# Kernel optimization log

Measured on AMD Instinct MI355X. Metric: run time of the kernel, lower is better.

## Reference

```python
import jax, jax.numpy as jnp
import numpy as np
from jax import lax

B, T, V = 128, 256, 64
HF = 32   # MLP feature-imputation hidden
CTX = 32  # context hidden
HID = 64  # LSTM hidden


def _uniform(k, shape, fan):
    s = 1.0 / np.sqrt(fan)
    return jax.random.uniform(k, shape, jnp.float32, -s, s)


def setup_inputs():
    key = jax.random.key(0)
    ks = jax.random.split(key, 40)
    values = jax.random.normal(ks[0], (B, T, V), jnp.float32)
    masks = (jax.random.uniform(ks[1], (B, T, V)) > 0.3).astype(jnp.float32)
    deltas = jax.random.uniform(ks[2], (B, T, V), jnp.float32) * 5.0
    lengths = jax.random.randint(ks[3], (B,), T // 2, T + 1)
    min_vals = jnp.min(values, axis=1, keepdims=True)
    max_vals = jnp.max(values, axis=1, keepdims=True)
    D_in = 2 * V + 2 * CTX
    return dict(
        lengths=lengths, values=values, masks=masks, deltas=deltas,
        min_vals=min_vals, max_vals=max_vals,
        W_decay=_uniform(ks[4], (V, V), V), b_decay=_uniform(ks[5], (V,), V),
        W_feat=_uniform(ks[6], (V, HF, V), V), b_feat=_uniform(ks[7], (V, HF), V),
        W_nl1=_uniform(ks[8], (HF, HF), HF), b_nl1=_uniform(ks[9], (HF,), HF),
        W_nl2=_uniform(ks[10], (1, HF), HF), b_nl2=_uniform(ks[11], (1,), HF),
        Wc1=_uniform(ks[12], (2 * CTX, 3 * V + 1), 3 * V + 1), bc1=_uniform(ks[13], (2 * CTX,), 3 * V + 1),
        Wc2=_uniform(ks[14], (CTX, 2 * CTX), 2 * CTX), bc2=_uniform(ks[15], (CTX,), 2 * CTX),
        W_ih_g=_uniform(ks[16], (3 * CTX, 2 * V), CTX), W_hh_g=_uniform(ks[17], (3 * CTX, CTX), CTX),
        b_ih_g=_uniform(ks[18], (3 * CTX,), CTX), b_hh_g=_uniform(ks[19], (3 * CTX,), CTX),
        W_init=_uniform(ks[20], (2 * HID, 2 * CTX), 2 * CTX), b_init=_uniform(ks[21], (2 * HID,), 2 * CTX),
        W_ih_f=_uniform(ks[22], (4 * HID, D_in), HID), W_hh_f=_uniform(ks[23], (4 * HID, HID), HID),
        b_ih_f=_uniform(ks[24], (4 * HID,), HID), b_hh_f=_uniform(ks[25], (4 * HID,), HID),
        W_ih_b=_uniform(ks[26], (4 * HID, D_in), HID), W_hh_b=_uniform(ks[27], (4 * HID, HID), HID),
        b_ih_b=_uniform(ks[28], (4 * HID,), HID), b_hh_b=_uniform(ks[29], (4 * HID,), HID),
        W_ri=_uniform(ks[30], (V, 2 * HID), 2 * HID), b_ri=_uniform(ks[31], (V,), 2 * HID),
        W_fu=_uniform(ks[32], (V, 2 * V), 2 * V), b_fu=_uniform(ks[33], (V,), 2 * V),
    )


def _gru(x, h, Wih, Whh, bih, bhh):
    gi = x @ Wih.T + bih
    gh = h @ Whh.T + bhh
    ir, iz, inn = jnp.split(gi, 3, axis=-1)
    hr, hz, hn = jnp.split(gh, 3, axis=-1)
    r = jax.nn.sigmoid(ir + hr)
    z = jax.nn.sigmoid(iz + hz)
    n = jnp.tanh(inn + r * hn)
    return (1.0 - z) * n + z * h


def _lstm(x, h, c, Wih, Whh, bih, bhh):
    g = x @ Wih.T + bih + h @ Whh.T + bhh
    i, f, gg, o = jnp.split(g, 4, axis=-1)
    c = jax.nn.sigmoid(f) * c + jax.nn.sigmoid(i) * jnp.tanh(gg)
    h = jax.nn.sigmoid(o) * jnp.tanh(c)
    return h, c


def _forward(lengths, values, masks, deltas, min_vals, max_vals,
             W_decay, b_decay, W_feat, b_feat, W_nl1, b_nl1, W_nl2, b_nl2,
             Wc1, bc1, Wc2, bc2, W_ih_g, W_hh_g, b_ih_g, b_hh_g,
             W_init, b_init, W_ih_f, W_hh_f, b_ih_f, b_hh_f,
             W_ih_b, W_hh_b, b_ih_b, b_hh_b, W_ri, b_ri, W_fu, b_fu):
    Bb, Tt, Vv = values.shape
    lf = lengths.astype(jnp.float32)
    pad = (jnp.arange(Tt)[None, :] + 1 <= lengths[:, None]).astype(jnp.float32)  # [B,T]

    msum = masks.sum(axis=1)                       # [B,V] observation counts
    means = values.sum(axis=1) / msum
    var = ((values - means[:, None, :]) ** 2).sum(axis=1) / (msum - 1.0)
    stdev = jnp.sqrt(var)
    missing = 1.0 - msum / lf[:, None]
    stats = jnp.concatenate([lf[:, None], means, stdev, missing], axis=1)  # [B,3V+1]

    mmn = jnp.maximum(max_vals - min_vals, 1e-8)   # [B,1,V]
    nv = (values - min_vals) / mmn
    nmeans = (means - min_vals[:, 0, :]) / mmn[:, 0, :]

    # last-observation-carried-forward x_prime
    nv_tm = jnp.swapaxes(nv, 0, 1)   # [T,B,V]
    m_tm = jnp.swapaxes(masks, 0, 1)

    def pstep(xp, xm):
        x_prev, m_prev = xm
        xp = m_prev * x_prev + (1.0 - m_prev) * xp
        return xp, xp
    _, xp_rest = lax.scan(pstep, nv_tm[0], (nv_tm[:-1], m_tm[:-1]))
    x_prime = jnp.swapaxes(jnp.concatenate([nv_tm[:1], xp_rest], axis=0), 0, 1)

    # InputTemporalDecay: F.linear(d, W*I, b) == d * diag(W) + b
    gamma = jnp.exp(-jax.nn.relu(deltas * jnp.diag(W_decay) + b_decay))
    x_decay = gamma * x_prime + (1.0 - gamma) * nmeans[:, None, :]
    x_complete = masks * nv + (1.0 - masks) * x_decay

    # context vectors
    ctx_mlp = jax.nn.relu(stats @ Wc1.T + bc1) @ Wc2.T + bc2  # [B,CTX]
    x_rnn_tm = jnp.swapaxes(jnp.concatenate([x_complete, masks], axis=-1), 0, 1)  # [T,B,2V]
    pad_tm = jnp.swapaxes(pad, 0, 1)[:, :, None]
    h0 = jnp.zeros((Bb, W_hh_g.shape[1]), values.dtype)

    def gstep(carry, inp):
        h, hn = carry
        x_t, p_t = inp
        h = _gru(x_t, h, W_ih_g, W_hh_g, b_ih_g, b_hh_g)
        hn = p_t * h + (1.0 - p_t) * hn
        return (h, hn), None
    (_, ctx_rnn), _ = lax.scan(gstep, (h0, h0), (x_rnn_tm, pad_tm))
    context = jnp.concatenate([ctx_mlp, ctx_rnn], axis=1)  # [B,2*CTX]

    hinit = context @ W_init.T + b_init  # [B,2H]
    cinit = jnp.tanh(hinit)
    Hh = hinit.shape[1] // 2
    hf0, hb0 = hinit[:, :Hh], hinit[:, Hh:]
    cf0, cb0 = cinit[:, :Hh], cinit[:, Hh:]

    ctx_bt = jnp.broadcast_to(context[:, None, :], (Bb, Tt, context.shape[1]))
    rnn_in_tm = jnp.swapaxes(jnp.concatenate([x_complete, masks, ctx_bt], axis=-1), 0, 1)  # [T,B,D]

    def fstep(carry, x):
        h, c = _lstm(x, carry[0], carry[1], W_ih_f, W_hh_f, b_ih_f, b_hh_f)
        return (h, c), h
    _, hf_rest = lax.scan(fstep, (hf0, cf0), rnn_in_tm[:-1])
    hf_all = jnp.concatenate([hf0[None], hf_rest], axis=0)  # [T,B,H]

    def bstep(carry, x):
        h, c = _lstm(x, carry[0], carry[1], W_ih_b, W_hh_b, b_ih_b, b_hh_b)
        return (h, c), h
    _, hb_rest = lax.scan(bstep, (hb0, cb0), rnn_in_tm[1:][::-1])  # t = T-1 .. 1
    hb_all = jnp.concatenate([hb0[None], hb_rest], axis=0)[::-1]   # time-aligned

    h_cat = jnp.concatenate([hf_all, hb_all], axis=-1)  # [T,B,2H]
    rnn_imp = jnp.swapaxes(h_cat @ W_ri.T + b_ri, 0, 1)  # [B,T,V]

    # per-variable masked feature imputation (no self-connection)
    eye = jnp.eye(Vv, dtype=values.dtype)
    Wm = W_feat * (1.0 - eye[:, None, :])                 # [V,HF,V]
    hidden = jnp.einsum('btv,ghv->btgh', x_complete, Wm) + b_feat  # [B,T,V,HF]
    z = jax.nn.relu(hidden) @ W_nl1.T + b_nl1
    feat_imp = (jax.nn.relu(z) @ W_nl2.T + b_nl2)[..., 0]  # [B,T,V]

    beta = jax.nn.sigmoid(jnp.concatenate([gamma, masks], axis=-1) @ W_fu.T + b_fu)
    final_imp = beta * feat_imp + (1.0 - beta) * rnn_imp

    # unnormalize all three estimates; stack as [3,B,T,V]
    out = jnp.stack([rnn_imp, feat_imp, final_imp], axis=0) * mmn[None] + min_vals[None]
    return out


def reference(lengths, values, masks, deltas, min_vals, max_vals,
              W_decay, b_decay, W_feat, b_feat, W_nl1, b_nl1, W_nl2, b_nl2,
              Wc1, bc1, Wc2, bc2, W_ih_g, W_hh_g, b_ih_g, b_hh_g,
              W_init, b_init, W_ih_f, W_hh_f, b_ih_f, b_hh_f,
              W_ih_b, W_hh_b, b_ih_b, b_hh_b, W_ri, b_ri, W_fu, b_fu):
    return _forward(lengths, values, masks, deltas, min_vals, max_vals,
                    W_decay, b_decay, W_feat, b_feat, W_nl1, b_nl1, W_nl2, b_nl2,
                    Wc1, bc1, Wc2, bc2, W_ih_g, W_hh_g, b_ih_g, b_hh_g,
                    W_init, b_init, W_ih_f, W_hh_f, b_ih_f, b_hh_f,
                    W_ih_b, W_hh_b, b_ih_b, b_hh_b, W_ri, b_ri, W_fu, b_fu)
```

## Files before the change

### kernel.cpp

```cpp
#include <hip/hip_runtime.h>
#include <hip/hip_fp16.h>

static constexpr int NB = 128;
static constexpr int NT = 256;
static constexpr int NV = 64;
static constexpr int NBT = NB * NT;
static constexpr int NBTV = NBT * NV;

typedef __attribute__((ext_vector_type(8))) short short8;
typedef __attribute__((ext_vector_type(4))) float f32x4;
typedef __attribute__((ext_vector_type(4))) float fvec4;

__device__ __forceinline__ void wave_lds_fence() {
    __builtin_amdgcn_sched_barrier(0);
    asm volatile("s_waitcnt lgkmcnt(0)" ::: "memory");
    __builtin_amdgcn_sched_barrier(0);
}

__device__ __forceinline__ void block_sync_lds() {
    __builtin_amdgcn_sched_barrier(0);
    asm volatile("s_waitcnt lgkmcnt(0)" ::: "memory");
    __builtin_amdgcn_s_barrier();
    asm volatile("" ::: "memory");
    __builtin_amdgcn_sched_barrier(0);
}

__device__ __forceinline__ unsigned short f2bf(float x) {
    unsigned int u = __float_as_uint(x);
    return (unsigned short)((u + 0x7FFFu + ((u >> 16) & 1u)) >> 16);
}
__device__ __forceinline__ float bf2f(unsigned short b) {
    return __uint_as_float(((unsigned int)b) << 16);
}
__device__ __forceinline__ unsigned short f2h(float x) {
    union { _Float16 h; unsigned short u; } c; c.h = (_Float16)x; return c.u;
}
__device__ __forceinline__ float fsigm(float x) {
    return __builtin_amdgcn_rcpf(1.0f + __expf(-x));
}
__device__ __forceinline__ float ftanh(float x) {
    return 1.0f - 2.0f * __builtin_amdgcn_rcpf(1.0f + __expf(2.0f * x));
}

__device__ __forceinline__ short8 pack8(float4 a, float4 b) {
    short8 r;
    r[0] = (short)f2bf(a.x); r[1] = (short)f2bf(a.y); r[2] = (short)f2bf(a.z); r[3] = (short)f2bf(a.w);
    r[4] = (short)f2bf(b.x); r[5] = (short)f2bf(b.y); r[6] = (short)f2bf(b.z); r[7] = (short)f2bf(b.w);
    return r;
}

__device__ __forceinline__ void dot4(float4& acc, const float4 wv, const float4 xv) {
    acc.x = fmaf(wv.x, xv.x, acc.x);
    acc.y = fmaf(wv.y, xv.y, acc.y);
    acc.z = fmaf(wv.z, xv.z, acc.z);
    acc.w = fmaf(wv.w, xv.w, acc.w);
}

__global__ __launch_bounds__(256) void k_prep(
    const float* __restrict__ Wf, const float* __restrict__ Wihf,
    const float* __restrict__ Wihb, const float* __restrict__ Wihg,
    const float* __restrict__ Whhf, const float* __restrict__ Whhb,
    const float* __restrict__ Whhg, const float* __restrict__ Wri,
    const float* __restrict__ Wfu,
    unsigned short* __restrict__ wbf, float* __restrict__ wdiag,
    unsigned short* __restrict__ wgf, unsigned short* __restrict__ wgb,
    unsigned short* __restrict__ wgg,
    unsigned short* __restrict__ whhf_h, unsigned short* __restrict__ whhb_h,
    unsigned short* __restrict__ whhg_h,
    unsigned short* __restrict__ wri_bf, unsigned short* __restrict__ wfu_bf,
    const int* __restrict__ lengths, const float* __restrict__ values,
    const float* __restrict__ masks, const float* __restrict__ minv,
    const float* __restrict__ maxv, float* __restrict__ stats,
    float* __restrict__ mmn_ws, float* __restrict__ nmeans_ws) {
    __shared__ float red[3][4][64];
    int bx = blockIdx.x;
    if (bx < 512) {
        int i = bx * 256 + threadIdx.x;
        if (i < NV * 32 * NV) wbf[i] = f2bf(Wf[i]);
        if (i < 2048) wdiag[i] = bf2f(f2bf(Wf[i * 64 + (i >> 5)]));
        if (i < 32768) {
            int n = i >> 7, k = i & 127;
            wgf[i] = f2bf(Wihf[n * 192 + k]);
            wgb[i] = f2bf(Wihb[n * 192 + k]);
        }
        if (i < 12288) wgg[i] = f2bf(Wihg[i]);
        if (i < 16384) { whhf_h[i] = f2h(Whhf[i]); whhb_h[i] = f2h(Whhb[i]); }
        if (i < 3072) whhg_h[i] = f2h(Whhg[i]);
        if (i < 8192) { wri_bf[i] = f2bf(Wri[i]); wfu_bf[i] = f2bf(Wfu[i]); }
    } else {
        int b = bx - 512; int tid = threadIdx.x;
        int v = tid & 63; int tc = tid >> 6;
        const float* vp = values + (size_t)b * NT * NV;
        const float* mp = masks + (size_t)b * NT * NV;
        float sv = 0.f, sq = 0.f, sm = 0.f;
        for (int t = tc; t < NT; t += 4) {
            float x = vp[t * NV + v]; float m = mp[t * NV + v];
            sv += x; sq += x * x; sm += m;
        }
        red[0][tc][v] = sv; red[1][tc][v] = sq; red[2][tc][v] = sm;
        __syncthreads();
        if (tc == 0) {
            sv = red[0][0][v] + red[0][1][v] + red[0][2][v] + red[0][3][v];
            sq = red[1][0][v] + red[1][1][v] + red[1][2][v] + red[1][3][v];
            sm = red[2][0][v] + red[2][1][v] + red[2][2][v] + red[2][3][v];
            float mean = sv / sm;
            float var = (sq - 2.0f * mean * sv + (float)NT * mean * mean) / (sm - 1.0f);
            var = fmaxf(var, 0.0f);
            float sd = sqrtf(var);
            float lf = (float)lengths[b];
            float miss = 1.0f - sm / lf;
            float mn = minv[b * NV + v]; float mx = maxv[b * NV + v];
            float mm = fmaxf(mx - mn, 1e-8f);
            float* st = stats + b * 256;
            if (v == 0) st[0] = lf;
            st[1 + v] = mean; st[65 + v] = sd; st[129 + v] = miss;
            mmn_ws[b * NV + v] = mm;
            nmeans_ws[b * NV + v] = (mean - mn) / mm;
        }
    }
}

__global__ __launch_bounds__(256) void k_fill(
    const float* __restrict__ values, const float* __restrict__ masks,
    const float* __restrict__ deltas, const float* __restrict__ minv,
    const float* __restrict__ Wd, const float* __restrict__ bd,
    const float* __restrict__ mmn_ws, const float* __restrict__ nmeans_ws,
    float* __restrict__ xcomp, float* __restrict__ gam) {
    int b = blockIdx.x; int tid = threadIdx.x;
    int v = tid & 63; int tc = tid >> 6;
    float mn = minv[b * NV + v];
    float mm = mmn_ws[b * NV + v];
    float nmean = nmeans_ws[b * NV + v];
    float wd = Wd[v * NV + v], bdv = bd[v];
    size_t base = (size_t)b * NT * NV + v;
    __shared__ float lastv[4][64];
    __shared__ int hasf[4][64];
    __shared__ float nv0s[64];
    int t0 = tc * 64;
    float last = 0.f; int has = 0;
    for (int t = t0; t < t0 + 64; t++) {
        float val = values[base + (size_t)t * NV];
        float m = masks[base + (size_t)t * NV];
        float nv = (val - mn) / mm;
        if (m != 0.f) { last = nv; has = 1; }
        if (tc == 0 && t == 0) nv0s[v] = nv;
    }
    lastv[tc][v] = last; hasf[tc][v] = has;
    __syncthreads();
    float xp = nv0s[v];
    for (int q = tc - 1; q >= 0; q--) {
        if (hasf[q][v]) { xp = lastv[q][v]; break; }
    }
    for (int t = t0; t < t0 + 64; t++) {
        size_t i = base + (size_t)t * NV;
        float val = values[i], m = masks[i], d = deltas[i];
        float nv = (val - mn) / mm;
        float g = expf(-fmaxf(fmaf(d, wd, bdv), 0.0f));
        float xd = g * xp + (1.0f - g) * nmean;
        float xc = m * nv + (1.0f - m) * xd;
        xcomp[i] = xc; gam[i] = g;
        xp = (m != 0.f) ? nv : xp;
    }
}

__global__ __launch_bounds__(256) void k_gates_g(
    const float* __restrict__ xcomp, const float* __restrict__ masks,
    const unsigned short* __restrict__ wgg, const float* __restrict__ bihg,
    float* __restrict__ gg) {
    int wave = threadIdx.x >> 6, lane = threadIdx.x & 63;
    int bt0 = blockIdx.x * 64 + wave * 16;
    int r = lane & 15, kc = lane >> 4;
    const float* xr = xcomp + (size_t)(bt0 + r) * NV + kc * 8;
    const float* mr = masks + (size_t)(bt0 + r) * NV + kc * 8;
    short8 af0 = pack8(*(const float4*)(xr), *(const float4*)(xr + 4));
    short8 af1 = pack8(*(const float4*)(xr + 32), *(const float4*)(xr + 36));
    short8 af2 = pack8(*(const float4*)(mr), *(const float4*)(mr + 4));
    short8 af3 = pack8(*(const float4*)(mr + 32), *(const float4*)(mr + 36));
    #pragma unroll 3
    for (int nt = 0; nt < 6; nt++) {
        const unsigned short* w = wgg + (size_t)(nt * 16 + r) * 128 + kc * 8;
        float bias = bihg[nt * 16 + r];
        f32x4 acc = {bias, bias, bias, bias};
        acc = __builtin_amdgcn_mfma_f32_16x16x32_bf16(af0, *(const short8*)(w), acc, 0, 0, 0);
        acc = __builtin_amdgcn_mfma_f32_16x16x32_bf16(af1, *(const short8*)(w + 32), acc, 0, 0, 0);
        acc = __builtin_amdgcn_mfma_f32_16x16x32_bf16(af2, *(const short8*)(w + 64), acc, 0, 0, 0);
        acc = __builtin_amdgcn_mfma_f32_16x16x32_bf16(af3, *(const short8*)(w + 96), acc, 0, 0, 0);
        #pragma unroll
        for (int i = 0; i < 4; i++)
            gg[(size_t)(bt0 + kc * 4 + i) * 96 + nt * 16 + r] = acc[i];
    }
}

#define GRU_STEP(T, GIN) { \
    const int t_ = (T); const int p_ = t_ & 1; \
    int4 raw_[4]; \
    const int4* hp_ = (const int4*)hsg[g][s]; \
    _Pragma("unroll") for (int q = 0; q < 4; q++) raw_[q] = hp_[q]; \
    const __half2* hhv_ = (const __half2*)raw_; \
    __half2 a0_ = zh2, a1_ = zh2, a2_ = zh2, a3_ = zh2; \
    _Pragma("unroll") for (int q = 0; q < 16; q += 4) { \
        a0_ = __hfma2(w2[q],     hhv_[q],     a0_); \
        a1_ = __hfma2(w2[q + 1], hhv_[q + 1], a1_); \
        a2_ = __hfma2(w2[q + 2], hhv_[q + 2], a2_); \
        a3_ = __hfma2(w2[q + 3], hhv_[q + 3], a3_); } \
    __half2 sA_ = __hadd2(__hadd2(a0_, a1_), __hadd2(a2_, a3_)); \
    float d_ = __low2float(sA_) + __high2float(sA_); \
    if (g < 2) { \
        gexg[p_][s][n][g] = GIN + bh + d_; \
    } else { \
        gexg[p_][s][n][2] = bh + d_; \
        gexg[p_][s][n][3] = GIN; \
    } \
    block_sync_lds(); \
    float qx_ = gexg[p_][s][n][0], qy_ = gexg[p_][s][n][1]; \
    float qz_ = gexg[p_][s][n][2], qw_ = gexg[p_][s][n][3]; \
    float rr_ = fsigm(qx_); \
    float zz_ = fsigm(qy_); \
    float nn_ = ftanh(qw_ + rr_ * qz_); \
    float h_ = (1.f - zz_) * nn_ + zz_ * hprev; \
    hprev = h_; \
    if (t_ < len) hn = h_; \
    hsg[g][s][n] = f2h(h_); \
    wave_lds_fence(); \
}

__global__ __launch_bounds__(256, 1) void k_mid(
    const float* __restrict__ gg_t, const int* __restrict__ lengths,
    const unsigned short* __restrict__ whhg_h, const float* __restrict__ bhh,
    float* __restrict__ ctx,
    const float* __restrict__ stats, const float* __restrict__ Wc1,
    const float* __restrict__ bc1, const float* __restrict__ Wc2,
    const float* __restrict__ bc2,
    const float* __restrict__ xcomp, const float* __restrict__ masks,
    const unsigned short* __restrict__ wbf,
    const float* __restrict__ wdiag, const float* __restrict__ bfeat,
    const float* __restrict__ Wnl1, const float* __restrict__ bnl1,
    const float* __restrict__ Wnl2, const float* __restrict__ bnl2,
    float* __restrict__ feat_out,
    const unsigned short* __restrict__ wgf, const unsigned short* __restrict__ wgb,
    float* __restrict__ gf, float* __restrict__ gb) {
    __shared__ __align__(16) unsigned short hsg[3][2][32];
    __shared__ __align__(16) float gexg[2][2][32][5];
    __shared__ __align__(16) float ss[193];
    __shared__ float h1[64];
    __shared__ __align__(16) unsigned short hbs[4][16 * 32];
    __shared__ __align__(16) float ldsx[4][64 * 16];
    __shared__ __align__(16) float fls[4][16 * 65];

    int bx = blockIdx.x;
    int tid = threadIdx.x;

    if (bx < 64) {
        int b0 = bx * 2;
        int g = tid >> 6;
        int lane = tid & 63;
        int s = lane >> 5, n = lane & 31;
        if (g == 3) {
            for (int t = 0; t < NT; t++) block_sync_lds();
            return;
        }
        int b = b0 + s;
        const __half2 zh2 = __float2half2_rn(0.f);
        int4 w4[4];
        {
            const int4* wp = (const int4*)(whhg_h + (size_t)(g * 32 + n) * 32);
            #pragma unroll
            for (int q = 0; q < 4; q++) w4[q] = wp[q];
        }
        const __half2* w2 = (const __half2*)w4;
        float bh = bhh[g * 32 + n];
        int len = lengths[b];
        float hprev = 0.f, hn = 0.f;
        hsg[g][s][n] = f2h(0.f);
        const float* gbase = gg_t + (size_t)b * NT * 96;
        #define GGIDX(T) ((size_t)(T) * 96 + g * 32 + n)
        float gi0 = gbase[GGIDX(0)];
        float gi1 = gbase[GGIDX(1)];
        float gi2 = gbase[GGIDX(2)];
        float gi3 = gbase[GGIDX(3)];
        wave_lds_fence();
        for (int t = 0; t < 252; t += 4) {
            GRU_STEP(t, gi0)
            gi0 = gbase[GGIDX(t + 4)];
            GRU_STEP(t + 1, gi1)
            gi1 = gbase[GGIDX(t + 5)];
            GRU_STEP(t + 2, gi2)
            gi2 = gbase[GGIDX(t + 6)];
            GRU_STEP(t + 3, gi3)
            gi3 = gbase[GGIDX(t + 7)];
        }
        GRU_STEP(252, gi0)
        GRU_STEP(253, gi1)
        GRU_STEP(254, gi2)
        GRU_STEP(255, gi3)
        #undef GGIDX
        if (g == 0) ctx[(b0 + s) * 64 + 32 + n] = hn;
    } else if (bx < 192) {
        if (tid >= 64) return;
        int b = bx - 64;
        ss[tid] = stats[b * 256 + tid];
        ss[64 + tid] = stats[b * 256 + 64 + tid];
        ss[128 + tid] = stats[b * 256 + 128 + tid];
        if (tid == 0) ss[192] = stats[b * 256 + 192];
        wave_lds_fence();
        float acc = bc1[tid];
        const float* w = Wc1 + (size_t)tid * 193;
        for (int k = 0; k < 193; k++) acc = fmaf(w[k], ss[k], acc);
        h1[tid] = fmaxf(acc, 0.f);
        wave_lds_fence();
        if (tid < 32) {
            float a = bc2[tid];
            const float* w2 = Wc2 + tid * 64;
            for (int k = 0; k < 64; k++) a = fmaf(w2[k], h1[k], a);
            ctx[b * 64 + tid] = a;
        }
    } else if (bx < 704) {
        int wave = tid >> 6; int lane = tid & 63;
        int bt0 = (bx - 192) * 64 + wave * 16;
        int r = lane & 15, kc = lane >> 4;
        unsigned short* hbw = hbs[wave];
        float* lx = ldsx[wave];
        float* flw = fls[wave];

        short8 a0, a1;
        {
            const float* xr = xcomp + (size_t)(bt0 + r) * NV + kc * 8;
            a0 = pack8(*(const float4*)(xr), *(const float4*)(xr + 4));
            a1 = pack8(*(const float4*)(xr + 32), *(const float4*)(xr + 36));
        }
        {
            int gc0 = kc * 16;
            const float* xr2 = xcomp + (size_t)(bt0 + r) * NV + gc0;
            #pragma unroll
            for (int e = 0; e < 16; e += 4) {
                float4 p = *(const float4*)(xr2 + e);
                lx[(gc0 + e + 0) * 16 + r] = bf2f(f2bf(p.x));
                lx[(gc0 + e + 1) * 16 + r] = bf2f(f2bf(p.y));
                lx[(gc0 + e + 2) * 16 + r] = bf2f(f2bf(p.z));
                lx[(gc0 + e + 3) * 16 + r] = bf2f(f2bf(p.w));
            }
        }
        short8 wb0, wb1;
        {
            const float* w = Wnl1 + r * 32 + kc * 8;
            wb0 = pack8(*(const float4*)w, *(const float4*)(w + 4));
            const float* w2 = Wnl1 + (16 + r) * 32 + kc * 8;
            wb1 = pack8(*(const float4*)w2, *(const float4*)(w2 + 4));
        }
        float b0i[4], b1i[4], w2a[4], w2b[4];
        #pragma unroll
        for (int i = 0; i < 4; i++) {
            b0i[i] = bnl1[kc * 4 + i];
            b1i[i] = bnl1[16 + kc * 4 + i];
            w2a[i] = Wnl2[kc * 4 + i];
            w2b[i] = Wnl2[16 + kc * 4 + i];
        }
        float bn2 = bnl2[0];
        __builtin_amdgcn_wave_barrier();

        #pragma unroll 2
        for (int g = 0; g < 64; g++) {
            __builtin_amdgcn_wave_barrier();
            float xv[4];
            #pragma unroll
            for (int i = 0; i < 4; i++) xv[i] = lx[g * 16 + kc * 4 + i];
            #pragma unroll
            for (int f = 0; f < 2; f++) {
                int n0 = g * 32 + f * 16;
                const unsigned short* wrow = wbf + (size_t)(n0 + r) * 64;
                short8 b0 = *(const short8*)(wrow + kc * 8);
                short8 b1 = *(const short8*)(wrow + 32 + kc * 8);
                f32x4 acc = {0.f, 0.f, 0.f, 0.f};
                acc = __builtin_amdgcn_mfma_f32_16x16x32_bf16(a0, b0, acc, 0, 0, 0);
                acc = __builtin_amdgcn_mfma_f32_16x16x32_bf16(a1, b1, acc, 0, 0, 0);
                int n = n0 + r;
                float wd = wdiag[n], bs = bfeat[n];
                #pragma unroll
                for (int i = 0; i < 4; i++) {
                    float h = acc[i] - xv[i] * wd + bs;
                    h = fmaxf(h, 0.0f);
                    hbw[(kc * 4 + i) * 32 + f * 16 + r] = f2bf(h);
                }
            }
            __builtin_amdgcn_wave_barrier();
            short8 ah = *(const short8*)(hbw + r * 32 + kc * 8);
            f32x4 zt0 = {0.f, 0.f, 0.f, 0.f}, zt1 = {0.f, 0.f, 0.f, 0.f};
            zt0 = __builtin_amdgcn_mfma_f32_16x16x32_bf16(wb0, ah, zt0, 0, 0, 0);
            zt1 = __builtin_amdgcn_mfma_f32_16x16x32_bf16(wb1, ah, zt1, 0, 0, 0);
            float p = 0.f;
            #pragma unroll
            for (int i = 0; i < 4; i++) {
                p = fmaf(fmaxf(zt0[i] + b0i[i], 0.0f), w2a[i], p);
                p = fmaf(fmaxf(zt1[i] + b1i[i], 0.0f), w2b[i], p);
            }
            p += __shfl_xor(p, 16, 64);
            p += __shfl_xor(p, 32, 64);
            if (lane < 16) flw[lane * 65 + g] = p + bn2;
        }
        __builtin_amdgcn_wave_barrier();
        #pragma unroll
        for (int q = 0; q < 16; q++)
            feat_out[(size_t)(bt0 + q) * NV + lane] = flw[q * 65 + lane];
    } else {
        int wave = tid >> 6, lane = tid & 63;
        int bt0 = (bx - 704) * 64 + wave * 16;
        int r = lane & 15, kc = lane >> 4;
        const float* xr = xcomp + (size_t)(bt0 + r) * NV + kc * 8;
        const float* mr = masks + (size_t)(bt0 + r) * NV + kc * 8;
        short8 af0 = pack8(*(const float4*)(xr), *(const float4*)(xr + 4));
        short8 af1 = pack8(*(const float4*)(xr + 32), *(const float4*)(xr + 36));
        short8 af2 = pack8(*(const float4*)(mr), *(const float4*)(mr + 4));
        short8 af3 = pack8(*(const float4*)(mr + 32), *(const float4*)(mr + 36));
        #pragma unroll 4
        for (int nt = 0; nt < 16; nt++) {
            const unsigned short* w = wgf + (size_t)(nt * 16 + r) * 128 + kc * 8;
            f32x4 acc = {0.f, 0.f, 0.f, 0.f};
            acc = __builtin_amdgcn_mfma_f32_16x16x32_bf16(af0, *(const short8*)(w), acc, 0, 0, 0);
            acc = __builtin_amdgcn_mfma_f32_16x16x32_bf16(af1, *(const short8*)(w + 32), acc, 0, 0, 0);
            acc = __builtin_amdgcn_mfma_f32_16x16x32_bf16(af2, *(const short8*)(w + 64), acc, 0, 0, 0);
            acc = __builtin_amdgcn_mfma_f32_16x16x32_bf16(af3, *(const short8*)(w + 96), acc, 0, 0, 0);
            int col = nt * 16 + r, g = col >> 6, n = col & 63;
            #pragma unroll
            for (int i = 0; i < 4; i++)
                gf[((size_t)(bt0 + kc * 4 + i) * 64 + n) * 4 + g] = acc[i];
        }
        #pragma unroll 4
        for (int nt = 0; nt < 16; nt++) {
            const unsigned short* w = wgb + (size_t)(nt * 16 + r) * 128 + kc * 8;
            f32x4 acc = {0.f, 0.f, 0.f, 0.f};
            acc = __builtin_amdgcn_mfma_f32_16x16x32_bf16(af0, *(const short8*)(w), acc, 0, 0, 0);
            acc = __builtin_amdgcn_mfma_f32_16x16x32_bf16(af1, *(const short8*)(w + 32), acc, 0, 0, 0);
            acc = __builtin_amdgcn_mfma_f32_16x16x32_bf16(af2, *(const short8*)(w + 64), acc, 0, 0, 0);
            acc = __builtin_amdgcn_mfma_f32_16x16x32_bf16(af3, *(const short8*)(w + 96), acc, 0, 0, 0);
            int col = nt * 16 + r, g = col >> 6, n = col & 63;
            #pragma unroll
            for (int i = 0; i < 4; i++)
                gb[((size_t)(bt0 + kc * 4 + i) * 64 + n) * 4 + g] = acc[i];
        }
    }
}

__global__ __launch_bounds__(256) void k_hc(
    const float* __restrict__ ctx, const float* __restrict__ Wi,
    const float* __restrict__ bi, float* __restrict__ hinit,
    const float* __restrict__ Wihf, const float* __restrict__ Wihb,
    const float* __restrict__ bihf, const float* __restrict__ bhhf,
    const float* __restrict__ bihb, const float* __restrict__ bhhb,
    float* __restrict__ ct_out) {
    __shared__ __align__(16) float sc[64];
    int bx = blockIdx.x; int tid = threadIdx.x;
    if (bx < 128) {
        int b = bx; int j = tid;
        if (j < 64) sc[j] = ctx[b * 64 + j];
        __syncthreads();
        if (j < 128) {
            const float4* w = (const float4*)(Wi + (size_t)j * 64);
            const float4* c4 = (const float4*)sc;
            float4 a = {0, 0, 0, 0};
            #pragma unroll
            for (int q = 0; q < 16; q++) dot4(a, w[q], c4[q]);
            hinit[b * 128 + j] = bi[j] + a.x + a.y + a.z + a.w;
        }
    } else {
        int bxx = bx - 128; int dir = bxx >> 7; int b = bxx & 127;
        int col = tid;
        if (col < 64) sc[col] = ctx[b * 64 + col];
        __syncthreads();
        const float* wc = (dir ? Wihb : Wihf) + (size_t)col * 192 + 128;
        float bias = dir ? (bihb[col] + bhhb[col]) : (bihf[col] + bhhf[col]);
        const float4* c4 = (const float4*)sc;
        float4 a = {0, 0, 0, 0};
        #pragma unroll
        for (int q = 0; q < 16; q++) dot4(a, *(const float4*)(wc + q * 4), c4[q]);
        int g = col >> 6, n = col & 63;
        ct_out[((size_t)bxx * 64 + n) * 4 + g] = bias + a.x + a.y + a.z + a.w;
    }
}

#define LSTM_STEP(S, GIN) { \
    const int s_ = (S); const int p_ = s_ & 1; \
    int4 raw_[8]; \
    const int4* hp_ = (const int4*)hs[g]; \
    _Pragma("unroll") for (int q = 0; q < 8; q++) raw_[q] = hp_[q]; \
    const __half2* hhv_ = (const __half2*)raw_; \
    __half2 a0_ = zh2, a1_ = zh2, a2_ = zh2, a3_ = zh2; \
    _Pragma("unroll") for (int q = 0; q < 32; q += 4) { \
        a0_ = __hfma2(w2[q],     hhv_[q],     a0_); \
        a1_ = __hfma2(w2[q + 1], hhv_[q + 1], a1_); \
        a2_ = __hfma2(w2[q + 2], hhv_[q + 2], a2_); \
        a3_ = __hfma2(w2[q + 3], hhv_[q + 3], a3_); } \
    __half2 sA_ = __hadd2(__hadd2(a0_, a1_), __hadd2(a2_, a3_)); \
    float d_ = __low2float(sA_) + __high2float(sA_); \
    gex[p_][n][g] = GIN + ctg + d_; \
    block_sync_lds(); \
    float qx_ = gex[p_][n][0], qy_ = gex[p_][n][1]; \
    float qz_ = gex[p_][n][2], qw_ = gex[p_][n][3]; \
    float ii_ = fsigm(qx_); \
    float ff_ = fsigm(qy_); \
    float gv_ = ftanh(qz_); \
    float oo_ = fsigm(qw_); \
    c = ff_ * c + ii_ * gv_; \
    float hv_ = oo_ * ftanh(c); \
    if (g == 0) { \
        int tout_ = dir ? (NT - 2 - s_) : (s_ + 1); \
        hall[((size_t)b * NT + tout_) * NV + n] = hv_; \
    } \
    hs[g][n] = f2h(hv_); \
    wave_lds_fence(); \
}

__global__ __launch_bounds__(256, 1) void k_lstm(
    const float* __restrict__ gf, const float* __restrict__ gb,
    const float* __restrict__ cterm, const float* __restrict__ hinit,
    const unsigned short* __restrict__ whhf_h, const unsigned short* __restrict__ whhb_h,
    float* __restrict__ out0, float* __restrict__ out1) {
    int bx = blockIdx.x; int dir = bx >> 7; int b = bx & 127;
    int tid = threadIdx.x;
    int g = tid >> 6;
    int n = tid & 63;
    const float* gates = dir ? gb : gf;
    const unsigned short* wsrc = dir ? whhb_h : whhf_h;
    float* hall = dir ? out1 : out0;
    __shared__ __align__(16) unsigned short hs[4][64];
    __shared__ __align__(16) float gex[2][64][5];
    const __half2 zh2 = __float2half2_rn(0.f);
    int4 w4[8];
    {
        const int4* wp = (const int4*)(wsrc + (size_t)(g * 64 + n) * 64);
        #pragma unroll
        for (int q = 0; q < 8; q++) w4[q] = wp[q];
    }
    const __half2* w2 = (const __half2*)w4;
    float ctg = cterm[((size_t)bx * 64 + n) * 4 + g];
    float c;
    {
        float h0 = hinit[b * 128 + dir * 64 + n];
        c = ftanh(h0);
        hs[g][n] = f2h(h0);
        if (g == 0) {
            int t0 = dir ? (NT - 1) : 0;
            hall[((size_t)b * NT + t0) * NV + n] = h0;
        }
    }
    size_t gbase = (size_t)b * NT * 256;
    #define GIDX(S) (gbase + (size_t)(dir ? (NT - 1 - (S)) : (S)) * 256 + n * 4 + g)
    float gi0 = gates[GIDX(0)];
    float gi1 = gates[GIDX(1)];
    float gi2 = gates[GIDX(2)];
    float gi3 = gates[GIDX(3)];
    wave_lds_fence();
    for (int sx = 0; sx < 252; sx += 4) {
        LSTM_STEP(sx, gi0)
        gi0 = gates[GIDX(sx + 4)];
        LSTM_STEP(sx + 1, gi1)
        gi1 = gates[GIDX(sx + 5)];
        LSTM_STEP(sx + 2, gi2)
        gi2 = gates[GIDX(sx + 6)];
        LSTM_STEP(sx + 3, gi3)
        gi3 = gates[GIDX(sx + 7)];
    }
    LSTM_STEP(252, gi0)
    LSTM_STEP(253, gi1)
    LSTM_STEP(254, gi2)
    #undef GIDX
}

__global__ __launch_bounds__(256) void k_post(
    const float* __restrict__ gam, const float* __restrict__ masks,
    const unsigned short* __restrict__ wri_bf, const unsigned short* __restrict__ wfu_bf,
    const float* __restrict__ bri, const float* __restrict__ bfu,
    const float* __restrict__ mmn_ws, const float* __restrict__ minv,
    float* out0, float* out1, float* out2) {
    int wave = threadIdx.x >> 6, lane = threadIdx.x & 63;
    int bt0 = blockIdx.x * 64 + wave * 16;
    int r = lane & 15, kc = lane >> 4;
    int b = bt0 >> 8;
    const float* h0r = out0 + (size_t)(bt0 + r) * NV + kc * 8;
    const float* h1r = out1 + (size_t)(bt0 + r) * NV + kc * 8;
    const float* gr  = gam  + (size_t)(bt0 + r) * NV + kc * 8;
    const float* mr  = masks + (size_t)(bt0 + r) * NV + kc * 8;
    short8 A0 = pack8(*(const float4*)(h0r), *(const float4*)(h0r + 4));
    short8 A1 = pack8(*(const float4*)(h0r + 32), *(const float4*)(h0r + 36));
    short8 A2 = pack8(*(const float4*)(h1r), *(const float4*)(h1r + 4));
    short8 A3 = pack8(*(const float4*)(h1r + 32), *(const float4*)(h1r + 36));
    short8 G0 = pack8(*(const float4*)(gr), *(const float4*)(gr + 4));
    short8 G1 = pack8(*(const float4*)(gr + 32), *(const float4*)(gr + 36));
    short8 M0 = pack8(*(const float4*)(mr), *(const float4*)(mr + 4));
    short8 M1 = pack8(*(const float4*)(mr + 32), *(const float4*)(mr + 36));
    #pragma unroll
    for (int nt = 0; nt < 4; nt++) {
        int n = nt * 16 + r;
        const unsigned short* wr = wri_bf + (size_t)n * 128 + kc * 8;
        const unsigned short* wf = wfu_bf + (size_t)n * 128 + kc * 8;
        float bi = bri[n], bf_ = bfu[n];
        f32x4 racc = {bi, bi, bi, bi};
        f32x4 bacc = {bf_, bf_, bf_, bf_};
        racc = __builtin_amdgcn_mfma_f32_16x16x32_bf16(A0, *(const short8*)(wr), racc, 0, 0, 0);
        racc = __builtin_amdgcn_mfma_f32_16x16x32_bf16(A1, *(const short8*)(wr + 32), racc, 0, 0, 0);
        racc = __builtin_amdgcn_mfma_f32_16x16x32_bf16(A2, *(const short8*)(wr + 64), racc, 0, 0, 0);
        racc = __builtin_amdgcn_mfma_f32_16x16x32_bf16(A3, *(const short8*)(wr + 96), racc, 0, 0, 0);
        bacc = __builtin_amdgcn_mfma_f32_16x16x32_bf16(G0, *(const short8*)(wf), bacc, 0, 0, 0);
        bacc = __builtin_amdgcn_mfma_f32_16x16x32_bf16(G1, *(const short8*)(wf + 32), bacc, 0, 0, 0);
        bacc = __builtin_amdgcn_mfma_f32_16x16x32_bf16(M0, *(const short8*)(wf + 64), bacc, 0, 0, 0);
        bacc = __builtin_amdgcn_mfma_f32_16x16x32_bf16(M1, *(const short8*)(wf + 96), bacc, 0, 0, 0);
        float mm = mmn_ws[b * NV + n], mn = minv[b * NV + n];
        #pragma unroll
        for (int i = 0; i < 4; i++) {
            int row = bt0 + kc * 4 + i;
            size_t idx = (size_t)row * NV + n;
            float rn = racc[i];
            float beta = fsigm(bacc[i]);
            float ft = out2[idx];
            float fin = beta * ft + (1.0f - beta) * rn;
            out0[idx] = fmaf(rn, mm, mn);
            out1[idx] = fmaf(ft, mm, mn);
            out2[idx] = fmaf(fin, mm, mn);
        }
    }
}

extern "C" void kernel_launch(void* const* d_in, const int* in_sizes, int n_in,
                              void* d_out, int out_size, void* d_ws, size_t ws_size,
                              hipStream_t stream) {
    const int*   lengths  = (const int*)d_in[0];
    const float* values   = (const float*)d_in[1];
    const float* masks    = (const float*)d_in[2];
    const float* deltas   = (const float*)d_in[3];
    const float* min_vals = (const float*)d_in[4];
    const float* max_vals = (const float*)d_in[5];
    const float* W_decay  = (const float*)d_in[6];
    const float* b_decay  = (const float*)d_in[7];
    const float* W_feat   = (const float*)d_in[8];
    const float* b_feat   = (const float*)d_in[9];
    const float* W_nl1    = (const float*)d_in[10];
    const float* b_nl1    = (const float*)d_in[11];
    const float* W_nl2    = (const float*)d_in[12];
    const float* b_nl2    = (const float*)d_in[13];
    const float* Wc1      = (const float*)d_in[14];
    const float* bc1      = (const float*)d_in[15];
    const float* Wc2      = (const float*)d_in[16];
    const float* bc2      = (const float*)d_in[17];
    const float* W_ih_g   = (const float*)d_in[18];
    const float* W_hh_g   = (const float*)d_in[19];
    const float* b_ih_g   = (const float*)d_in[20];
    const float* b_hh_g   = (const float*)d_in[21];
    const float* W_init   = (const float*)d_in[22];
    const float* b_init   = (const float*)d_in[23];
    const float* W_ih_f   = (const float*)d_in[24];
    const float* W_hh_f   = (const float*)d_in[25];
    const float* b_ih_f   = (const float*)d_in[26];
    const float* b_hh_f   = (const float*)d_in[27];
    const float* W_ih_b   = (const float*)d_in[28];
    const float* W_hh_b   = (const float*)d_in[29];
    const float* b_ih_b   = (const float*)d_in[30];
    const float* b_hh_b   = (const float*)d_in[31];
    const float* W_ri     = (const float*)d_in[32];
    const float* b_ri     = (const float*)d_in[33];
    const float* W_fu     = (const float*)d_in[34];
    const float* b_fu     = (const float*)d_in[35];

    float* ws = (float*)d_ws;
    float* xcomp  = ws;
    float* gam    = ws + 2097152;
    unsigned short* wri_bf = (unsigned short*)(ws + 4194304);
    unsigned short* wfu_bf = (unsigned short*)(ws + 4198400);
    float* stats  = ws + 6291456;
    float* mmn    = ws + 6324224;
    float* nmeans = ws + 6332416;
    float* ctx    = ws + 6340608;
    float* hinit  = ws + 6348800;
    unsigned short* wbf = (unsigned short*)(ws + 6365184);
    float* wdiag  = ws + 6430720;
    unsigned short* wgf = (unsigned short*)(ws + 6432768);
    unsigned short* wgb = (unsigned short*)(ws + 6449152);
    unsigned short* wgg = (unsigned short*)(ws + 6465536);
    unsigned short* whhf_h = (unsigned short*)(ws + 6471680);
    unsigned short* whhb_h = (unsigned short*)(ws + 6479872);
    unsigned short* whhg_h = (unsigned short*)(ws + 6488064);
    float* cterm  = ws + 6489600;
    float* gates_f = ws + 6555136;
    float* gates_b = ws + 14943744;
    float* gates_g = ws + 23332352;

    float* out0 = (float*)d_out;
    float* out1 = out0 + NBTV;
    float* out2 = out0 + 2 * NBTV;

    k_prep<<<640, 256, 0, stream>>>(W_feat, W_ih_f, W_ih_b, W_ih_g, W_hh_f, W_hh_b, W_hh_g,
                                    W_ri, W_fu,
                                    wbf, wdiag, wgf, wgb, wgg, whhf_h, whhb_h, whhg_h,
                                    wri_bf, wfu_bf,
                                    lengths, values, masks, min_vals, max_vals, stats, mmn, nmeans);
    k_fill<<<NB, 256, 0, stream>>>(values, masks, deltas, min_vals, W_decay, b_decay, mmn, nmeans, xcomp, gam);
    k_gates_g<<<NBT / 64, 256, 0, stream>>>(xcomp, masks, wgg, b_ih_g, gates_g);
    k_mid<<<1216, 256, 0, stream>>>(gates_g, lengths, whhg_h, b_hh_g, ctx,
                                    stats, Wc1, bc1, Wc2, bc2,
                                    xcomp, masks, wbf, wdiag, b_feat, W_nl1, b_nl1, W_nl2, b_nl2, out2,
                                    wgf, wgb, gates_f, gates_b);
    k_hc<<<384, 256, 0, stream>>>(ctx, W_init, b_init, hinit,
                                  W_ih_f, W_ih_b, b_ih_f, b_hh_f, b_ih_b, b_hh_b, cterm);
    k_lstm<<<256, 256, 0, stream>>>(gates_f, gates_b, cterm, hinit, whhf_h, whhb_h, out0, out1);
    k_post<<<NBT / 64, 256, 0, stream>>>(gam, masks, wri_bf, wfu_bf, b_ri, b_fu, mmn, min_vals,
                                         out0, out1, out2);
}
```

Measured before the change: 307.2 us.

## Fold k_hc into LSTM and move half of feature MLP into LSTM launch

Removes the k_hc launch by computing the initial hidden state and context gate term inside each LSTM block. Half of the feature-imputation MLP blocks move from k_mid into extra blocks of the k_lstm grid, so they can fill CUs left idle by the 256 latency-bound LSTM blocks. This cuts one launch and shortens k_mid. The risk is that the larger LDS footprint in k_lstm and block scheduling order could delay the LSTM blocks.

New measurement: 285.4 us. -7.1%, faster.

```diff
diff --git a/kernel.cpp b/kernel.cpp
--- a/kernel.cpp
+++ b/kernel.cpp
@@ -224,6 +224,84 @@
     wave_lds_fence(); \
 }
 
+#define FEAT_BODY(BT0) { \
+    int bt0 = (BT0); \
+    int r = lane & 15, kc = lane >> 4; \
+    unsigned short* hbw = hbs[wave]; \
+    float* lx = ldsx[wave]; \
+    float* flw = fls[wave]; \
+    short8 a0, a1; \
+    { \
+        const float* xr = xcomp + (size_t)(bt0 + r) * NV + kc * 8; \
+        a0 = pack8(*(const float4*)(xr), *(const float4*)(xr + 4)); \
+        a1 = pack8(*(const float4*)(xr + 32), *(const float4*)(xr + 36)); \
+    } \
+    { \
+        int gc0 = kc * 16; \
+        const float* xr2 = xcomp + (size_t)(bt0 + r) * NV + gc0; \
+        _Pragma("unroll") for (int e = 0; e < 16; e += 4) { \
+            float4 p = *(const float4*)(xr2 + e); \
+            lx[(gc0 + e + 0) * 16 + r] = bf2f(f2bf(p.x)); \
+            lx[(gc0 + e + 1) * 16 + r] = bf2f(f2bf(p.y)); \
+            lx[(gc0 + e + 2) * 16 + r] = bf2f(f2bf(p.z)); \
+            lx[(gc0 + e + 3) * 16 + r] = bf2f(f2bf(p.w)); \
+        } \
+    } \
+    short8 wb0, wb1; \
+    { \
+        const float* w = Wnl1 + r * 32 + kc * 8; \
+        wb0 = pack8(*(const float4*)w, *(const float4*)(w + 4)); \
+        const float* w2p = Wnl1 + (16 + r) * 32 + kc * 8; \
+        wb1 = pack8(*(const float4*)w2p, *(const float4*)(w2p + 4)); \
+    } \
+    float b0i[4], b1i[4], w2a[4], w2b[4]; \
+    _Pragma("unroll") for (int i = 0; i < 4; i++) { \
+        b0i[i] = bnl1[kc * 4 + i]; \
+        b1i[i] = bnl1[16 + kc * 4 + i]; \
+        w2a[i] = Wnl2[kc * 4 + i]; \
+        w2b[i] = Wnl2[16 + kc * 4 + i]; \
+    } \
+    float bn2 = bnl2[0]; \
+    __builtin_amdgcn_wave_barrier(); \
+    _Pragma("unroll 2") for (int g = 0; g < 64; g++) { \
+        __builtin_amdgcn_wave_barrier(); \
+        float xv[4]; \
+        _Pragma("unroll") for (int i = 0; i < 4; i++) xv[i] = lx[g * 16 + kc * 4 + i]; \
+        _Pragma("unroll") for (int f = 0; f < 2; f++) { \
+            int n0 = g * 32 + f * 16; \
+            const unsigned short* wrow = wbf + (size_t)(n0 + r) * 64; \
+            short8 b0 = *(const short8*)(wrow + kc * 8); \
+            short8 b1 = *(const short8*)(wrow + 32 + kc * 8); \
+            f32x4 acc = {0.f, 0.f, 0.f, 0.f}; \
+            acc = __builtin_amdgcn_mfma_f32_16x16x32_bf16(a0, b0, acc, 0, 0, 0); \
+            acc = __builtin_amdgcn_mfma_f32_16x16x32_bf16(a1, b1, acc, 0, 0, 0); \
+            int n = n0 + r; \
+            float wd = wdiag[n], bs = bfeat[n]; \
+            _Pragma("unroll") for (int i = 0; i < 4; i++) { \
+                float h = acc[i] - xv[i] * wd + bs; \
+                h = fmaxf(h, 0.0f); \
+                hbw[(kc * 4 + i) * 32 + f * 16 + r] = f2bf(h); \
+            } \
+        } \
+        __builtin_amdgcn_wave_barrier(); \
+        short8 ah = *(const short8*)(hbw + r * 32 + kc * 8); \
+        f32x4 zt0 = {0.f, 0.f, 0.f, 0.f}, zt1 = {0.f, 0.f, 0.f, 0.f}; \
+        zt0 = __builtin_amdgcn_mfma_f32_16x16x32_bf16(wb0, ah, zt0, 0, 0, 0); \
+        zt1 = __builtin_amdgcn_mfma_f32_16x16x32_bf16(wb1, ah, zt1, 0, 0, 0); \
+        float p = 0.f; \
+        _Pragma("unroll") for (int i = 0; i < 4; i++) { \
+            p = fmaf(fmaxf(zt0[i] + b0i[i], 0.0f), w2a[i], p); \
+            p = fmaf(fmaxf(zt1[i] + b1i[i], 0.0f), w2b[i], p); \
+        } \
+        p += __shfl_xor(p, 16, 64); \
+        p += __shfl_xor(p, 32, 64); \
+        if (lane < 16) flw[lane * 65 + g] = p + bn2; \
+    } \
+    __builtin_amdgcn_wave_barrier(); \
+    _Pragma("unroll") for (int q = 0; q < 16; q++) \
+        feat_out[(size_t)(bt0 + q) * NV + lane] = flw[q * 65 + lane]; \
+}
+
 __global__ __launch_bounds__(256, 1) void k_mid(
     const float* __restrict__ gg_t, const int* __restrict__ lengths,
     const unsigned short* __restrict__ whhg_h, const float* __restrict__ bhh,
@@ -314,96 +392,12 @@
             for (int k = 0; k < 64; k++) a = fmaf(w2[k], h1[k], a);
             ctx[b * 64 + tid] = a;
         }
-    } else if (bx < 704) {
+    } else if (bx < 448) {
         int wave = tid >> 6; int lane = tid & 63;
-        int bt0 = (bx - 192) * 64 + wave * 16;
-        int r = lane & 15, kc = lane >> 4;
-        unsigned short* hbw = hbs[wave];
-        float* lx = ldsx[wave];
-        float* flw = fls[wave];
-
-        short8 a0, a1;
-        {
-            const float* xr = xcomp + (size_t)(bt0 + r) * NV + kc * 8;
-            a0 = pack8(*(const float4*)(xr), *(const float4*)(xr + 4));
-            a1 = pack8(*(const float4*)(xr + 32), *(const float4*)(xr + 36));
-        }
-        {
-            int gc0 = kc * 16;
-            const float* xr2 = xcomp + (size_t)(bt0 + r) * NV + gc0;
-            #pragma unroll
-            for (int e = 0; e < 16; e += 4) {
-                float4 p = *(const float4*)(xr2 + e);
-                lx[(gc0 + e + 0) * 16 + r] = bf2f(f2bf(p.x));
-                lx[(gc0 + e + 1) * 16 + r] = bf2f(f2bf(p.y));
-                lx[(gc0 + e + 2) * 16 + r] = bf2f(f2bf(p.z));
-                lx[(gc0 + e + 3) * 16 + r] = bf2f(f2bf(p.w));
-            }
-        }
-        short8 wb0, wb1;
-        {
-            const float* w = Wnl1 + r * 32 + kc * 8;
-            wb0 = pack8(*(const float4*)w, *(const float4*)(w + 4));
-            const float* w2 = Wnl1 + (16 + r) * 32 + kc * 8;
-            wb1 = pack8(*(const float4*)w2, *(const float4*)(w2 + 4));
-        }
-        float b0i[4], b1i[4], w2a[4], w2b[4];
-        #pragma unroll
-        for (int i = 0; i < 4; i++) {
-            b0i[i] = bnl1[kc * 4 + i];
-            b1i[i] = bnl1[16 + kc * 4 + i];
-            w2a[i] = Wnl2[kc * 4 + i];
-            w2b[i] = Wnl2[16 + kc * 4 + i];
-        }
-        float bn2 = bnl2[0];
-        __builtin_amdgcn_wave_barrier();
-
-        #pragma unroll 2
-        for (int g = 0; g < 64; g++) {
-            __builtin_amdgcn_wave_barrier();
-            float xv[4];
-            #pragma unroll
-            for (int i = 0; i < 4; i++) xv[i] = lx[g * 16 + kc * 4 + i];
-            #pragma unroll
-            for (int f = 0; f < 2; f++) {
-                int n0 = g * 32 + f * 16;
-                const unsigned short* wrow = wbf + (size_t)(n0 + r) * 64;
-                short8 b0 = *(const short8*)(wrow + kc * 8);
-                short8 b1 = *(const short8*)(wrow + 32 + kc * 8);
-                f32x4 acc = {0.f, 0.f, 0.f, 0.f};
-                acc = __builtin_amdgcn_mfma_f32_16x16x32_bf16(a0, b0, acc, 0, 0, 0);
-                acc = __builtin_amdgcn_mfma_f32_16x16x32_bf16(a1, b1, acc, 0, 0, 0);
-                int n = n0 + r;
-                float wd = wdiag[n], bs = bfeat[n];
-                #pragma unroll
-                for (int i = 0; i < 4; i++) {
-                    float h = acc[i] - xv[i] * wd + bs;
-                    h = fmaxf(h, 0.0f);
-                    hbw[(kc * 4 + i) * 32 + f * 16 + r] = f2bf(h);
-                }
-            }
-            __builtin_amdgcn_wave_barrier();
-            short8 ah = *(const short8*)(hbw + r * 32 + kc * 8);
-            f32x4 zt0 = {0.f, 0.f, 0.f, 0.f}, zt1 = {0.f, 0.f, 0.f, 0.f};
-            zt0 = __builtin_amdgcn_mfma_f32_16x16x32_bf16(wb0, ah, zt0, 0, 0, 0);
-            zt1 = __builtin_amdgcn_mfma_f32_16x16x32_bf16(wb1, ah, zt1, 0, 0, 0);
-            float p = 0.f;
-            #pragma unroll
-            for (int i = 0; i < 4; i++) {
-                p = fmaf(fmaxf(zt0[i] + b0i[i], 0.0f), w2a[i], p);
-                p = fmaf(fmaxf(zt1[i] + b1i[i], 0.0f), w2b[i], p);
-            }
-            p += __shfl_xor(p, 16, 64);
-            p += __shfl_xor(p, 32, 64);
-            if (lane < 16) flw[lane * 65 + g] = p + bn2;
-        }
-        __builtin_amdgcn_wave_barrier();
-        #pragma unroll
-        for (int q = 0; q < 16; q++)
-            feat_out[(size_t)(bt0 + q) * NV + lane] = flw[q * 65 + lane];
+        FEAT_BODY((bx - 192) * 64 + wave * 16)
     } else {
         int wave = tid >> 6, lane = tid & 63;
-        int bt0 = (bx - 704) * 64 + wave * 16;
+        int bt0 = (bx - 448) * 64 + wave * 16;
         int r = lane & 15, kc = lane >> 4;
         const float* xr = xcomp + (size_t)(bt0 + r) * NV + kc * 8;
         const float* mr = masks + (size_t)(bt0 + r) * NV + kc * 8;
@@ -437,43 +431,6 @@
             for (int i = 0; i < 4; i++)
                 gb[((size_t)(bt0 + kc * 4 + i) * 64 + n) * 4 + g] = acc[i];
         }
-    }
-}
-
-__global__ __launch_bounds__(256) void k_hc(
-    const float* __restrict__ ctx, const float* __restrict__ Wi,
-    const float* __restrict__ bi, float* __restrict__ hinit,
-    const float* __restrict__ Wihf, const float* __restrict__ Wihb,
-    const float* __restrict__ bihf, const float* __restrict__ bhhf,
-    const float* __restrict__ bihb, const float* __restrict__ bhhb,
-    float* __restrict__ ct_out) {
-    __shared__ __align__(16) float sc[64];
-    int bx = blockIdx.x; int tid = threadIdx.x;
-    if (bx < 128) {
-        int b = bx; int j = tid;
-        if (j < 64) sc[j] = ctx[b * 64 + j];
-        __syncthreads();
-        if (j < 128) {
-            const float4* w = (const float4*)(Wi + (size_t)j * 64);
-            const float4* c4 = (const float4*)sc;
-            float4 a = {0, 0, 0, 0};
-            #pragma unroll
-            for (int q = 0; q < 16; q++) dot4(a, w[q], c4[q]);
-            hinit[b * 128 + j] = bi[j] + a.x + a.y + a.z + a.w;
-        }
-    } else {
-        int bxx = bx - 128; int dir = bxx >> 7; int b = bxx & 127;
-        int col = tid;
-        if (col < 64) sc[col] = ctx[b * 64 + col];
-        __syncthreads();
-        const float* wc = (dir ? Wihb : Wihf) + (size_t)col * 192 + 128;
-        float bias = dir ? (bihb[col] + bhhb[col]) : (bihf[col] + bhhf[col]);
-        const float4* c4 = (const float4*)sc;
-        float4 a = {0, 0, 0, 0};
-        #pragma unroll
-        for (int q = 0; q < 16; q++) dot4(a, *(const float4*)(wc + q * 4), c4[q]);
-        int g = col >> 6, n = col & 63;
-        ct_out[((size_t)bxx * 64 + n) * 4 + g] = bias + a.x + a.y + a.z + a.w;
     }
 }
 
@@ -511,18 +468,41 @@
 
 __global__ __launch_bounds__(256, 1) void k_lstm(
     const float* __restrict__ gf, const float* __restrict__ gb,
-    const float* __restrict__ cterm, const float* __restrict__ hinit,
+    const float* __restrict__ ctx,
     const unsigned short* __restrict__ whhf_h, const unsigned short* __restrict__ whhb_h,
-    float* __restrict__ out0, float* __restrict__ out1) {
-    int bx = blockIdx.x; int dir = bx >> 7; int b = bx & 127;
+    const float* __restrict__ Wihf, const float* __restrict__ Wihb,
+    const float* __restrict__ bihf, const float* __restrict__ bhhf,
+    const float* __restrict__ bihb, const float* __restrict__ bhhb,
+    const float* __restrict__ Wini, const float* __restrict__ bini,
+    float* __restrict__ out0, float* __restrict__ out1,
+    const float* __restrict__ xcomp, const unsigned short* __restrict__ wbf,
+    const float* __restrict__ wdiag, const float* __restrict__ bfeat,
+    const float* __restrict__ Wnl1, const float* __restrict__ bnl1,
+    const float* __restrict__ Wnl2, const float* __restrict__ bnl2,
+    float* __restrict__ feat_out) {
+    __shared__ __align__(16) unsigned short hs[4][64];
+    __shared__ __align__(16) float gex[2][64][5];
+    __shared__ __align__(16) float sctx[64];
+    __shared__ __align__(16) float sh0[64];
+    __shared__ __align__(16) unsigned short hbs[4][16 * 32];
+    __shared__ __align__(16) float ldsx[4][64 * 16];
+    __shared__ __align__(16) float fls[4][16 * 65];
+
+    int bx = blockIdx.x;
     int tid = threadIdx.x;
+
+    if (bx >= 256) {
+        int wave = tid >> 6; int lane = tid & 63;
+        FEAT_BODY((bx - 256) * 64 + 16384 + wave * 16)
+        return;
+    }
+
+    int dir = bx >> 7; int b = bx & 127;
     int g = tid >> 6;
     int n = tid & 63;
     const float* gates = dir ? gb : gf;
     const unsigned short* wsrc = dir ? whhb_h : whhf_h;
     float* hall = dir ? out1 : out0;
-    __shared__ __align__(16) unsigned short hs[4][64];
-    __shared__ __align__(16) float gex[2][64][5];
     const __half2 zh2 = __float2half2_rn(0.f);
     int4 w4[8];
     {
@@ -531,23 +511,43 @@
         for (int q = 0; q < 8; q++) w4[q] = wp[q];
     }
     const __half2* w2 = (const __half2*)w4;
-    float ctg = cterm[((size_t)bx * 64 + n) * 4 + g];
-    float c;
-    {
-        float h0 = hinit[b * 128 + dir * 64 + n];
-        c = ftanh(h0);
-        hs[g][n] = f2h(h0);
-        if (g == 0) {
-            int t0 = dir ? (NT - 1) : 0;
-            hall[((size_t)b * NT + t0) * NV + n] = h0;
-        }
-    }
     size_t gbase = (size_t)b * NT * 256;
     #define GIDX(S) (gbase + (size_t)(dir ? (NT - 1 - (S)) : (S)) * 256 + n * 4 + g)
     float gi0 = gates[GIDX(0)];
     float gi1 = gates[GIDX(1)];
     float gi2 = gates[GIDX(2)];
     float gi3 = gates[GIDX(3)];
+    if (tid < 64) sctx[tid] = ctx[b * 64 + tid];
+    __syncthreads();
+    float ctg;
+    {
+        const float4* wc = (const float4*)((dir ? Wihb : Wihf) + (size_t)tid * 192 + 128);
+        float bias = dir ? (bihb[tid] + bhhb[tid]) : (bihf[tid] + bhhf[tid]);
+        const float4* c4 = (const float4*)sctx;
+        float4 a = {0, 0, 0, 0};
+        #pragma unroll
+        for (int q = 0; q < 16; q++) dot4(a, wc[q], c4[q]);
+        ctg = bias + a.x + a.y + a.z + a.w;
+    }
+    if (tid < 64) {
+        const float4* wi = (const float4*)(Wini + (size_t)(dir * 64 + tid) * 64);
+        const float4* c4 = (const float4*)sctx;
+        float4 a = {0, 0, 0, 0};
+        #pragma unroll
+        for (int q = 0; q < 16; q++) dot4(a, wi[q], c4[q]);
+        sh0[tid] = bini[dir * 64 + tid] + a.x + a.y + a.z + a.w;
+    }
+    __syncthreads();
+    float c;
+    {
+        float h0 = sh0[n];
+        c = ftanh(h0);
+        hs[g][n] = f2h(h0);
+        if (g == 0) {
+            int t0 = dir ? (NT - 1) : 0;
+            hall[((size_t)b * NT + t0) * NV + n] = h0;
+        }
+    }
     wave_lds_fence();
     for (int sx = 0; sx < 252; sx += 4) {
         LSTM_STEP(sx, gi0)
@@ -668,7 +668,6 @@
     float* mmn    = ws + 6324224;
     float* nmeans = ws + 6332416;
     float* ctx    = ws + 6340608;
-    float* hinit  = ws + 6348800;
     unsigned short* wbf = (unsigned short*)(ws + 6365184);
     float* wdiag  = ws + 6430720;
     unsigned short* wgf = (unsigned short*)(ws + 6432768);
@@ -677,7 +676,6 @@
     unsigned short* whhf_h = (unsigned short*)(ws + 6471680);
     unsigned short* whhb_h = (unsigned short*)(ws + 6479872);
     unsigned short* whhg_h = (unsigned short*)(ws + 6488064);
-    float* cterm  = ws + 6489600;
     float* gates_f = ws + 6555136;
     float* gates_b = ws + 14943744;
     float* gates_g = ws + 23332352;
@@ -693,13 +691,14 @@
                                     lengths, values, masks, min_vals, max_vals, stats, mmn, nmeans);
     k_fill<<<NB, 256, 0, stream>>>(values, masks, deltas, min_vals, W_decay, b_decay, mmn, nmeans, xcomp, gam);
     k_gates_g<<<NBT / 64, 256, 0, stream>>>(xcomp, masks, wgg, b_ih_g, gates_g);
-    k_mid<<<1216, 256, 0, stream>>>(gates_g, lengths, whhg_h, b_hh_g, ctx,
-                                    stats, Wc1, bc1, Wc2, bc2,
-                                    xcomp, masks, wbf, wdiag, b_feat, W_nl1, b_nl1, W_nl2, b_nl2, out2,
-                                    wgf, wgb, gates_f, gates_b);
-    k_hc<<<384, 256, 0, stream>>>(ctx, W_init, b_init, hinit,
-                                  W_ih_f, W_ih_b, b_ih_f, b_hh_f, b_ih_b, b_hh_b, cterm);
-    k_lstm<<<256, 256, 0, stream>>>(gates_f, gates_b, cterm, hinit, whhf_h, whhb_h, out0, out1);
+    k_mid<<<960, 256, 0, stream>>>(gates_g, lengths, whhg_h, b_hh_g, ctx,
+                                   stats, Wc1, bc1, Wc2, bc2,
+                                   xcomp, masks, wbf, wdiag, b_feat, W_nl1, b_nl1, W_nl2, b_nl2, out2,
+                                   wgf, wgb, gates_f, gates_b);
+    k_lstm<<<512, 256, 0, stream>>>(gates_f, gates_b, ctx, whhf_h, whhb_h,
+                                    W_ih_f, W_ih_b, b_ih_f, b_hh_f, b_ih_b, b_hh_b,
+                                    W_init, b_init, out0, out1,
+                                    xcomp, wbf, wdiag, b_feat, W_nl1, b_nl1, W_nl2, b_nl2, out2);
     k_post<<<NBT / 64, 256, 0, stream>>>(gam, masks, wri_bf, wfu_bf, b_ri, b_fu, mmn, min_vals,
                                          out0, out1, out2);
 }
```
